# Optimization experiments

Measured on AMD Instinct MI355X. Metric: run time of the kernel, lower is better.

Reference implementation:

```python
import jax, jax.numpy as jnp
import numpy as np

B, C = 4096, 1024  # batch_size, label_size (== embedding_dim of dense outputs)


def setup_inputs() -> dict:
    key = jax.random.key(0)
    k1, k2, k3 = jax.random.split(key, 3)
    return {
        "outs": jax.random.normal(k1, (B, C), dtype=jnp.float32),
        "class_centers": jax.random.normal(k2, (C, C), dtype=jnp.float32),
        "batch_label": jax.random.randint(k3, (B,), 0, C, dtype=jnp.int32),
    }


def reference(outs, class_centers, batch_label):
    b, c = outs.shape
    # ---- standard cross-entropy (F.cross_entropy, mean reduction) ----
    logp = jax.nn.log_softmax(outs, axis=-1)
    ce = -jnp.mean(jnp.take_along_axis(logp, batch_label[:, None].astype(jnp.int32), axis=1))

    # ---- InfoNCE with Wasserstein hard-negative mining ----
    # memory bank stores detached embeddings -> centers carry no gradient
    centers = jax.lax.stop_gradient(class_centers)
    pos = centers[batch_label]  # [B, C] positive per anchor

    # calculate_2_wasserstein_dist on 1-D vectors reduces EXACTLY to
    # ||x - y||^2 - 2*d*sqrt(1e-15)  (covariance terms vanish for a single column)
    const = jnp.float32(-2.0 * c * np.sqrt(1e-15))
    x = jax.lax.stop_gradient(outs)  # similarity used only for index selection
    sq = jnp.sum(x * x, axis=-1)  # [B]
    sim = sq[:, None] + sq[None, :] - 2.0 * (x @ x.T) + const  # [B, B]

    # negatives: different label (self automatically excluded: same label)
    mask = batch_label[:, None] != batch_label[None, :]  # [B, B]
    neg_inf = jnp.float32(-1e30)
    # hard negative: largest wasserstein distance among negatives (topk k=1)
    hard_idx = jnp.argmax(jnp.where(mask, sim, neg_inf), axis=1)  # [B]
    # random negative: uniform over negatives via Gumbel-max (torch randperm analogue)
    g = jax.random.gumbel(jax.random.key(42), (b, b), dtype=jnp.float32)
    rand_idx = jnp.argmax(jnp.where(mask, g, neg_inf), axis=1)  # [B]

    pos_sim = jnp.sum(outs * pos, axis=-1)                # [B]
    n_rand = jnp.sum(outs * outs[rand_idx], axis=-1)      # [B]
    n_hard = jnp.sum(outs * outs[hard_idx], axis=-1)      # [B]
    logits = jnp.stack([pos_sim, n_rand, n_hard], axis=1)  # [B, 1+num_negatives]
    info_nce = -jnp.mean(jax.nn.log_softmax(logits, axis=1)[:, 0])

    return ce + 0.1 * info_nce
```

## Files before the change

### kernel.cpp

```cpp
#include <hip/hip_runtime.h>
#include <hip/hip_bf16.h>
#include <stdint.h>

#define Bsz 4096
#define Csz 1024

typedef __attribute__((ext_vector_type(8))) short short8;
typedef __attribute__((ext_vector_type(4))) float f32x4;

__device__ __forceinline__ unsigned fenc(float v) {
  unsigned u = __float_as_uint(v);
  return (u & 0x80000000u) ? ~u : (u | 0x80000000u);
}

__device__ __forceinline__ void load_lds16(const void* g, void* l) {
  __builtin_amdgcn_global_load_lds(
      (const __attribute__((address_space(1))) void*)g,
      (__attribute__((address_space(3))) void*)l, 16, 0, 0);
}

__device__ __forceinline__ uint32_t rotl32(uint32_t x, int r) {
  return (x << r) | (x >> (32 - r));
}

__global__ __launch_bounds__(256) void k_rowstats(
    const float* __restrict__ outs, const int* __restrict__ label,
    unsigned short* __restrict__ xb, float* __restrict__ sq,
    float* __restrict__ ce) {
  const int row = blockIdx.x;
  const int tid = threadIdx.x;
  const int lane = tid & 63, wid = tid >> 6;
  const float4 v = reinterpret_cast<const float4*>(outs + (size_t)row * Csz)[tid];

  ushort4 u4;
  {
    __hip_bfloat16 h;
    h = __float2bfloat16(v.x); u4.x = *reinterpret_cast<const unsigned short*>(&h);
    h = __float2bfloat16(v.y); u4.y = *reinterpret_cast<const unsigned short*>(&h);
    h = __float2bfloat16(v.z); u4.z = *reinterpret_cast<const unsigned short*>(&h);
    h = __float2bfloat16(v.w); u4.w = *reinterpret_cast<const unsigned short*>(&h);
  }
  reinterpret_cast<ushort4*>(xb + (size_t)row * Csz)[tid] = u4;

  __shared__ float wred[3][4];
  float mx = fmaxf(fmaxf(v.x, v.y), fmaxf(v.z, v.w));
#pragma unroll
  for (int off = 32; off; off >>= 1) mx = fmaxf(mx, __shfl_xor(mx, off, 64));
  if (lane == 0) wred[0][wid] = mx;
  __syncthreads();
  mx = fmaxf(fmaxf(wred[0][0], wred[0][1]), fmaxf(wred[0][2], wred[0][3]));

  float se = expf(v.x - mx) + expf(v.y - mx) + expf(v.z - mx) + expf(v.w - mx);
  float s2 = v.x * v.x + v.y * v.y + v.z * v.z + v.w * v.w;
#pragma unroll
  for (int off = 32; off; off >>= 1) {
    se += __shfl_xor(se, off, 64);
    s2 += __shfl_xor(s2, off, 64);
  }
  if (lane == 0) { wred[1][wid] = se; wred[2][wid] = s2; }
  __syncthreads();
  if (tid == 0) {
    const float set = wred[1][0] + wred[1][1] + wred[1][2] + wred[1][3];
    const float sqt = wred[2][0] + wred[2][1] + wred[2][2] + wred[2][3];
    sq[row] = sqt;
    ce[row] = -(outs[(size_t)row * Csz + label[row]] - mx - logf(set));
  }
}

__global__ __launch_bounds__(256) void k_hard(
    const unsigned short* __restrict__ xb, const float* __restrict__ sq,
    const int* __restrict__ label, unsigned long long* __restrict__ hard) {
  __shared__ unsigned short As[128 * 64];
  __shared__ unsigned short Bs[128 * 64];
  const int bi = blockIdx.x >> 5, bj = blockIdx.x & 31;
  const int tid = threadIdx.x;
  const int wid = tid >> 6, lane = tid & 63;
  const int wr = wid >> 1, wc = wid & 1;

  f32x4 acc[4][4];
#pragma unroll
  for (int m = 0; m < 4; ++m)
#pragma unroll
    for (int n = 0; n < 4; ++n) acc[m][n] = (f32x4){0.f, 0.f, 0.f, 0.f};

  const unsigned short* Ag = xb + (size_t)(bi * 128) * Csz;
  const unsigned short* Bg = xb + (size_t)(bj * 128) * Csz;
  const int lrow = lane >> 3;
  const int lch = (lane & 7) * 8;

  for (int kt = 0; kt < Csz; kt += 64) {
#pragma unroll
    for (int c = 0; c < 4; ++c) {
      const int r = wid * 32 + c * 8;
      load_lds16(Ag + (size_t)(r + lrow) * Csz + kt + lch, &As[r * 64]);
      load_lds16(Bg + (size_t)(r + lrow) * Csz + kt + lch, &Bs[r * 64]);
    }
    __syncthreads();
#pragma unroll
    for (int ks = 0; ks < 2; ++ks) {
      const int kb = ks * 32 + (lane >> 4) * 8;
      short8 a[4], b[4];
#pragma unroll
      for (int m = 0; m < 4; ++m)
        a[m] = *reinterpret_cast<const short8*>(
            &As[(wr * 64 + m * 16 + (lane & 15)) * 64 + kb]);
#pragma unroll
      for (int n = 0; n < 4; ++n)
        b[n] = *reinterpret_cast<const short8*>(
            &Bs[(wc * 64 + n * 16 + (lane & 15)) * 64 + kb]);
#pragma unroll
      for (int m = 0; m < 4; ++m)
#pragma unroll
        for (int n = 0; n < 4; ++n)
          acc[m][n] = __builtin_amdgcn_mfma_f32_16x16x32_bf16(a[m], b[n], acc[m][n], 0, 0, 0);
    }
    __syncthreads();
  }

  const float cst = -2.0f * 1024.0f * 3.1622776601683794e-8f;
#pragma unroll
  for (int m = 0; m < 4; ++m) {
#pragma unroll
    for (int r = 0; r < 4; ++r) {
      const int i = bi * 128 + wr * 64 + m * 16 + (lane >> 4) * 4 + r;
      const int li = label[i];
      const float sqi = sq[i];
      float bestv = -3.0e38f;
      int bestj = 0x7FFFFFFF;
#pragma unroll
      for (int n = 0; n < 4; ++n) {
        const int j = bj * 128 + wc * 64 + n * 16 + (lane & 15);
        const float val = sqi + sq[j] - 2.0f * acc[m][n][r] + cst;
        if (label[j] != li && val > bestv) { bestv = val; bestj = j; }
      }
      unsigned long long pack =
          (bestj == 0x7FFFFFFF)
              ? 0ull
              : (((unsigned long long)fenc(bestv)) << 32) | (unsigned)(~bestj);
#pragma unroll
      for (int off = 1; off < 16; off <<= 1) {
        unsigned long long o = __shfl_xor(pack, off, 64);
        if (o > pack) pack = o;
      }
      if ((lane & 15) == 0 && pack) atomicMax(&hard[i], pack);
    }
  }
}

__global__ __launch_bounds__(256) void k_rand(
    const int* __restrict__ label, int* __restrict__ ridx) {
  const int i = blockIdx.x;
  const int tid = threadIdx.x;
  const int lane = tid & 63, wid = tid >> 6;
  const int li0 = label[i], li1 = label[i + 2048];
  const uint32_t k1c = 42u, k2c = 0x1BD11BDAu ^ 42u;
  unsigned long long b0 = 0ull, b1 = 0ull;
  for (int j = tid; j < Bsz; j += 256) {
    uint32_t x0 = (uint32_t)(i * Bsz + j);
    uint32_t x1 = x0 + 8388608u;
    x1 += k1c;
#define RND(rt) { x0 += x1; x1 = rotl32(x1, rt); x1 ^= x0; }
    RND(13) RND(15) RND(26) RND(6)
    x0 += k1c; x1 += k2c + 1u;
    RND(17) RND(29) RND(16) RND(24)
    x0 += k2c; x1 += 2u;
    RND(13) RND(15) RND(26) RND(6)
    x1 += k1c + 3u;
    RND(17) RND(29) RND(16) RND(24)
    x0 += k1c; x1 += k2c + 4u;
    RND(13) RND(15) RND(26) RND(6)
    x0 += k2c; x1 += 5u;
#undef RND
    const int lj = label[j];
    if (lj != li0) {
      unsigned long long p = (((unsigned long long)(x0 >> 9)) << 32) | (uint32_t)(~j);
      if (p > b0) b0 = p;
    }
    if (lj != li1) {
      unsigned long long p = (((unsigned long long)(x1 >> 9)) << 32) | (uint32_t)(~j);
      if (p > b1) b1 = p;
    }
  }
#pragma unroll
  for (int off = 32; off; off >>= 1) {
    unsigned long long o0 = __shfl_xor(b0, off, 64); if (o0 > b0) b0 = o0;
    unsigned long long o1 = __shfl_xor(b1, off, 64); if (o1 > b1) b1 = o1;
  }
  __shared__ unsigned long long r0[4], r1[4];
  if (lane == 0) { r0[wid] = b0; r1[wid] = b1; }
  __syncthreads();
  if (tid == 0) {
#pragma unroll
    for (int w = 1; w < 4; ++w) {
      if (r0[w] > b0) b0 = r0[w];
      if (r1[w] > b1) b1 = r1[w];
    }
    ridx[i] = (int)(~(uint32_t)b0);
    ridx[i + 2048] = (int)(~(uint32_t)b1);
  }
}

__global__ __launch_bounds__(256) void k_nce(
    const float* __restrict__ outs, const float* __restrict__ centers,
    const int* __restrict__ label, const unsigned long long* __restrict__ hard,
    const int* __restrict__ ridx, float* __restrict__ nce) {
  const int i = blockIdx.x;
  const int tid = threadIdx.x;
  const int lane = tid & 63, wid = tid >> 6;
  const int li = label[i];
  const int jh = (int)(~(uint32_t)hard[i]);
  const int jr = ridx[i];
  const float4 a  = reinterpret_cast<const float4*>(outs + (size_t)i * Csz)[tid];
  const float4 c  = reinterpret_cast<const float4*>(centers + (size_t)li * Csz)[tid];
  const float4 rr = reinterpret_cast<const float4*>(outs + (size_t)jr * Csz)[tid];
  const float4 hh = reinterpret_cast<const float4*>(outs + (size_t)jh * Csz)[tid];
  float dp = a.x * c.x + a.y * c.y + a.z * c.z + a.w * c.w;
  float dr = a.x * rr.x + a.y * rr.y + a.z * rr.z + a.w * rr.w;
  float dh = a.x * hh.x + a.y * hh.y + a.z * hh.z + a.w * hh.w;
#pragma unroll
  for (int off = 32; off; off >>= 1) {
    dp += __shfl_xor(dp, off, 64);
    dr += __shfl_xor(dr, off, 64);
    dh += __shfl_xor(dh, off, 64);
  }
  __shared__ float w0[4], w1[4], w2[4];
  if (lane == 0) { w0[wid] = dp; w1[wid] = dr; w2[wid] = dh; }
  __syncthreads();
  if (tid == 0) {
    const float l0 = w0[0] + w0[1] + w0[2] + w0[3];
    const float l1 = w1[0] + w1[1] + w1[2] + w1[3];
    const float l2 = w2[0] + w2[1] + w2[2] + w2[3];
    const float m = fmaxf(l0, fmaxf(l1, l2));
    const float lse = logf(expf(l0 - m) + expf(l1 - m) + expf(l2 - m));
    nce[i] = -(l0 - m - lse);
  }
}

__global__ __launch_bounds__(1024) void k_final(
    const float* __restrict__ ce, const float* __restrict__ nce,
    float* __restrict__ out) {
  __shared__ double s[1024];
  const int tid = threadIdx.x;
  double v = 0.0;
#pragma unroll
  for (int q = 0; q < 4; ++q) {
    v += (double)ce[tid + q * 1024];
    v += 0.1 * (double)nce[tid + q * 1024];
  }
  s[tid] = v;
  __syncthreads();
  for (int off = 512; off; off >>= 1) {
    if (tid < off) s[tid] += s[tid + off];
    __syncthreads();
  }
  if (tid == 0) out[0] = (float)(s[0] / 4096.0);
}

extern "C" void kernel_launch(void* const* d_in, const int* in_sizes, int n_in,
                              void* d_out, int out_size, void* d_ws, size_t ws_size,
                              hipStream_t stream) {
  const float* outs = (const float*)d_in[0];
  const float* centers = (const float*)d_in[1];
  const int* label = (const int*)d_in[2];
  float* out = (float*)d_out;

  char* ws = (char*)d_ws;
  unsigned short* xb = (unsigned short*)ws;
  unsigned long long* hard = (unsigned long long*)(ws + (8u << 20));
  float* sq = (float*)(ws + (8u << 20) + 32768);
  float* ce = sq + Bsz;
  float* nce = ce + Bsz;
  int* ridx = (int*)(nce + Bsz);

  hipMemsetAsync(hard, 0, Bsz * sizeof(unsigned long long), stream);
  k_rowstats<<<Bsz, 256, 0, stream>>>(outs, label, xb, sq, ce);
  k_hard<<<1024, 256, 0, stream>>>(xb, sq, label, hard);
  k_rand<<<Bsz / 2, 256, 0, stream>>>(label, ridx);
  k_nce<<<Bsz, 256, 0, stream>>>(outs, centers, label, hard, ridx, nce);
  k_final<<<1, 1024, 0, stream>>>(ce, nce, out);
}
```

Before: 179.2 us.

## Exploit Gram matrix symmetry in hard-negative kernel and swizzle LDS layout

The hard-negative GEMM now computes only upper-triangular 128x128 tiles (528 blocks instead of 1024). Each off-diagonal tile also runs a column-wise argmax and writes it to the transposed rows, so the symmetric half of x·xᵀ is never recomputed. The LDS tiles are also XOR-swizzled by row to reduce bank conflicts on the MFMA fragment loads. The costs are a triangular index decode loop, an extra epilogue with more atomics per tile, and fewer blocks to spread across CUs.

```diff
diff --git a/kernel.cpp b/kernel.cpp
--- a/kernel.cpp
+++ b/kernel.cpp
@@ -72,10 +72,17 @@
     const int* __restrict__ label, unsigned long long* __restrict__ hard) {
   __shared__ unsigned short As[128 * 64];
   __shared__ unsigned short Bs[128 * 64];
-  const int bi = blockIdx.x >> 5, bj = blockIdx.x & 31;
+
+  int rem = blockIdx.x, bi = 0;
+  while (rem >= 32 - bi) { rem -= 32 - bi; ++bi; }
+  const int bj = bi + rem;
+
   const int tid = threadIdx.x;
   const int wid = tid >> 6, lane = tid & 63;
   const int wr = wid >> 1, wc = wid & 1;
+  const int fr = lane & 15;
+  const int fq = lane >> 4;
+  const int sx = lane & 7;
 
   f32x4 acc[4][4];
 #pragma unroll
@@ -86,7 +93,7 @@
   const unsigned short* Ag = xb + (size_t)(bi * 128) * Csz;
   const unsigned short* Bg = xb + (size_t)(bj * 128) * Csz;
   const int lrow = lane >> 3;
-  const int lch = (lane & 7) * 8;
+  const int lch = ((lane & 7) ^ lrow) * 8;
 
   for (int kt = 0; kt < Csz; kt += 64) {
 #pragma unroll
@@ -98,16 +105,16 @@
     __syncthreads();
 #pragma unroll
     for (int ks = 0; ks < 2; ++ks) {
-      const int kb = ks * 32 + (lane >> 4) * 8;
+      const int choff = ((ks * 4 + fq) ^ sx) * 8;
       short8 a[4], b[4];
 #pragma unroll
       for (int m = 0; m < 4; ++m)
         a[m] = *reinterpret_cast<const short8*>(
-            &As[(wr * 64 + m * 16 + (lane & 15)) * 64 + kb]);
+            &As[(wr * 64 + m * 16 + fr) * 64 + choff]);
 #pragma unroll
       for (int n = 0; n < 4; ++n)
         b[n] = *reinterpret_cast<const short8*>(
-            &Bs[(wc * 64 + n * 16 + (lane & 15)) * 64 + kb]);
+            &Bs[(wc * 64 + n * 16 + fr) * 64 + choff]);
 #pragma unroll
       for (int m = 0; m < 4; ++m)
 #pragma unroll
@@ -118,18 +125,19 @@
   }
 
   const float cst = -2.0f * 1024.0f * 3.1622776601683794e-8f;
+
 #pragma unroll
   for (int m = 0; m < 4; ++m) {
 #pragma unroll
     for (int r = 0; r < 4; ++r) {
-      const int i = bi * 128 + wr * 64 + m * 16 + (lane >> 4) * 4 + r;
+      const int i = bi * 128 + wr * 64 + m * 16 + fq * 4 + r;
       const int li = label[i];
       const float sqi = sq[i];
       float bestv = -3.0e38f;
       int bestj = 0x7FFFFFFF;
 #pragma unroll
       for (int n = 0; n < 4; ++n) {
-        const int j = bj * 128 + wc * 64 + n * 16 + (lane & 15);
+        const int j = bj * 128 + wc * 64 + n * 16 + fr;
         const float val = sqi + sq[j] - 2.0f * acc[m][n][r] + cst;
         if (label[j] != li && val > bestv) { bestv = val; bestj = j; }
       }
@@ -142,7 +150,34 @@
         unsigned long long o = __shfl_xor(pack, off, 64);
         if (o > pack) pack = o;
       }
-      if ((lane & 15) == 0 && pack) atomicMax(&hard[i], pack);
+      if (fr == 0 && pack) atomicMax(&hard[i], pack);
+    }
+  }
+
+  if (bi != bj) {
+#pragma unroll
+    for (int n = 0; n < 4; ++n) {
+      const int j = bj * 128 + wc * 64 + n * 16 + fr;
+      const int lj = label[j];
+      const float sqj = sq[j];
+      unsigned long long pack = 0ull;
+#pragma unroll
+      for (int m = 0; m < 4; ++m) {
+#pragma unroll
+        for (int r = 0; r < 4; ++r) {
+          const int i = bi * 128 + wr * 64 + m * 16 + fq * 4 + r;
+          if (label[i] != lj) {
+            const float val = sq[i] + sqj - 2.0f * acc[m][n][r] + cst;
+            const unsigned long long p =
+                (((unsigned long long)fenc(val)) << 32) | (unsigned)(~i);
+            if (p > pack) pack = p;
+          }
+        }
+      }
+      unsigned long long o;
+      o = __shfl_xor(pack, 16, 64); if (o > pack) pack = o;
+      o = __shfl_xor(pack, 32, 64); if (o > pack) pack = o;
+      if (fq == 0 && pack) atomicMax(&hard[j], pack);
     }
   }
 }
@@ -274,7 +309,7 @@
 
   hipMemsetAsync(hard, 0, Bsz * sizeof(unsigned long long), stream);
   k_rowstats<<<Bsz, 256, 0, stream>>>(outs, label, xb, sq, ce);
-  k_hard<<<1024, 256, 0, stream>>>(xb, sq, label, hard);
+  k_hard<<<528, 256, 0, stream>>>(xb, sq, label, hard);
   k_rand<<<Bsz / 2, 256, 0, stream>>>(label, ridx);
   k_nce<<<Bsz, 256, 0, stream>>>(outs, centers, label, hard, ridx, nce);
   k_final<<<1, 1024, 0, stream>>>(ce, nce, out);
```

Measured after the change: 171.9 us. 4.1% less time.
